# Performance work log

Measured on AMD Instinct MI355X. Metric: run time of the kernel, lower is better.

The kernel has to match this reference:

```python
import jax, jax.numpy as jnp
import numpy as np

D_MODEL = 2048
NUM_HEADS = 16
HEAD_DIM = D_MODEL // NUM_HEADS
LAYER_IDX = 0
NUM_LAYERS = 13
REINIT_LAMBDA = 0.8


def setup_inputs() -> dict:
    key = jax.random.key(0)
    ks = jax.random.split(key, 8)
    B, S = 2, 2048
    x = jax.random.normal(ks[0], (B, S, D_MODEL), dtype=jnp.float32)
    init = 1.0 / np.sqrt(D_MODEL)
    def w(k):
        return jax.random.uniform(k, (D_MODEL, D_MODEL), dtype=jnp.float32, minval=-init, maxval=init)
    lam_init = REINIT_LAMBDA * ((LAYER_IDX + 1) / NUM_LAYERS)
    return {
        "x": x,
        "q1_w": w(ks[1]), "k1_w": w(ks[2]),
        "q2_w": w(ks[3]), "k2_w": w(ks[4]),
        "v_w": w(ks[5]), "o_w": w(ks[6]),
        "lambda_param": jnp.full((NUM_HEADS,), lam_init, dtype=jnp.float32),
    }


def _heads(t, B, S):
    # [B, S, D] -> [B, H, S, Dh]
    return t.reshape(B, S, NUM_HEADS, HEAD_DIM).transpose(0, 2, 1, 3)


def reference(x, q1_w, k1_w, q2_w, k2_w, v_w, o_w, lambda_param):
    B, S, _ = x.shape
    # nn.Linear(bias=False): y = x @ W.T, W is [out, in]
    q1 = _heads(x @ q1_w.T, B, S)
    k1 = _heads(x @ k1_w.T, B, S)
    q2 = _heads(x @ q2_w.T, B, S)
    k2 = _heads(x @ k2_w.T, B, S)
    v = _heads(x @ v_w.T, B, S)
    scale = jnp.sqrt(jnp.float32(HEAD_DIM))
    attn1 = jax.nn.softmax(jnp.einsum('bhqd,bhkd->bhqk', q1, k1) / scale, axis=-1)
    attn2 = jax.nn.softmax(jnp.einsum('bhqd,bhkd->bhqk', q2, k2) / scale, axis=-1)
    lam = lambda_param.reshape(1, NUM_HEADS, 1, 1)
    out = jnp.einsum('bhqk,bhkd->bhqd', attn1 - lam * attn2, v)
    out = out.transpose(0, 2, 1, 3).reshape(B, S, D_MODEL)
    return out @ o_w.T
```

## Files before the change

kernel.cpp:

```cpp
#include <hip/hip_runtime.h>
#include <hip/hip_bf16.h>
#include <stdint.h>

typedef __bf16 bf16_t;
typedef __bf16 bf16x8 __attribute__((ext_vector_type(8)));
typedef float f32x4 __attribute__((ext_vector_type(4)));

#define D_MODEL 2048
#define SEQ     2048
#define NHEADS  16
#define HDIM    128
#define BATCH   2
#define NTOK    (BATCH * SEQ)
#define NELEM   ((size_t)BATCH * SEQ * D_MODEL)
#define D2      ((size_t)D_MODEL * D_MODEL)

__global__ void __launch_bounds__(256)
cvt7_kernel(const float* __restrict__ x,
            const float* __restrict__ w0, const float* __restrict__ w1,
            const float* __restrict__ w2, const float* __restrict__ w3,
            const float* __restrict__ w4, const float* __restrict__ w5,
            bf16_t* __restrict__ xb, bf16_t* __restrict__ wb) {
  const int y = blockIdx.y;
  const float* srcs[7] = {x, w0, w1, w2, w3, w4, w5};
  const float* src = srcs[y];
  bf16_t* dst = (y == 0) ? xb : wb + (size_t)(y - 1) * D2;
  const size_t n = (y == 0) ? NELEM : D2;
  const size_t base = ((size_t)blockIdx.x * 256 + threadIdx.x) * 8;
  if (base >= n) return;
  f32x4 lo = *(const f32x4*)(src + base);
  f32x4 hi = *(const f32x4*)(src + base + 4);
  union { bf16x8 v; bf16_t h[8]; } u;
#pragma unroll
  for (int j = 0; j < 4; j++) {
    u.h[j]     = (bf16_t)lo[j];
    u.h[j + 4] = (bf16_t)hi[j];
  }
  *(bf16x8*)(dst + base) = u.v;
}

__device__ __forceinline__ void async_load16(const void* g, void* l) {
  __builtin_amdgcn_global_load_lds(
      (const __attribute__((address_space(1))) void*)g,
      (__attribute__((address_space(3))) void*)l, 16, 0, 0);
}

template <int TRANS, typename TC>
__device__ __forceinline__ void gemm_tile_body(const bf16_t* __restrict__ A,
                                               const bf16_t* __restrict__ W,
                                               TC* __restrict__ C) {
  extern __shared__ char smem[];
  bf16_t* As = (bf16_t*)smem;
  bf16_t* Bs = (bf16_t*)smem + 128 * 32;
  const int K = D_MODEL, N = D_MODEL;
  const int tid  = threadIdx.x;
  const int wave = tid >> 6, lane = tid & 63;
  const int quad = lane >> 4, l16 = lane & 15;
  const int tm = blockIdx.x * 128, tn = blockIdx.y * 128;
  const int wm = (wave & 1) * 64, wn = (wave >> 1) * 64;

  f32x4 acc[4][4];
#pragma unroll
  for (int i = 0; i < 4; i++)
#pragma unroll
    for (int j = 0; j < 4; j++) acc[i][j] = (f32x4){0.f, 0.f, 0.f, 0.f};

  const int srow = lane >> 2;
  const int scol = (lane & 3) * 8;

  for (int k0 = 0; k0 < K; k0 += 32) {
    __syncthreads();
#pragma unroll
    for (int i = 0; i < 2; i++) {
      const int rbase = (i * 4 + wave) * 16;
      async_load16(A + (size_t)(tm + rbase + srow) * K + k0 + scol, As + rbase * 32);
      async_load16(W + (size_t)(tn + rbase + srow) * K + k0 + scol, Bs + rbase * 32);
    }
    __syncthreads();

    bf16x8 af[4], bfr[4];
#pragma unroll
    for (int i = 0; i < 4; i++)
      af[i] = *(const bf16x8*)(As + (wm + i * 16 + l16) * 32 + quad * 8);
#pragma unroll
    for (int j = 0; j < 4; j++)
      bfr[j] = *(const bf16x8*)(Bs + (wn + j * 16 + l16) * 32 + quad * 8);
#pragma unroll
    for (int i = 0; i < 4; i++)
#pragma unroll
      for (int j = 0; j < 4; j++)
        acc[i][j] = __builtin_amdgcn_mfma_f32_16x16x32_bf16(af[i], bfr[j], acc[i][j], 0, 0, 0);
  }

#pragma unroll
  for (int i = 0; i < 4; i++) {
    const int r0 = wm + i * 16 + quad * 4;
#pragma unroll
    for (int j = 0; j < 4; j++) {
      const int c = tn + wn + j * 16 + l16;
      if constexpr (TRANS) {
        const int m = tm + r0;
        const int b = m >> 11;
        const int s = m & (SEQ - 1);
        union { bf16_t h[4]; uint2 u2; } p;
#pragma unroll
        for (int r = 0; r < 4; r++) p.h[r] = (bf16_t)acc[i][j][r];
        *(uint2*)((bf16_t*)C + (size_t)(b * D_MODEL + c) * SEQ + s) = p.u2;
      } else {
#pragma unroll
        for (int r = 0; r < 4; r++)
          C[(size_t)(tm + r0 + r) * N + c] = (TC)acc[i][j][r];
      }
    }
  }
}

__global__ void __launch_bounds__(256)
gemm_out_kernel(const bf16_t* __restrict__ A, const bf16_t* __restrict__ W,
                float* __restrict__ C) {
  gemm_tile_body<0, float>(A, W, C);
}

template <int TRANS, typename TC>
__device__ __forceinline__ void gemm256_body(const bf16_t* __restrict__ A,
                                             const bf16_t* __restrict__ W,
                                             TC* __restrict__ C,
                                             const int tm, const int tn) {
  extern __shared__ char smem[];
  constexpr int K = D_MODEL;
  constexpr int NT = K / 64;
  const int tid = threadIdx.x;
  const int wid = tid >> 6, lane = tid & 63;
  const int quad = lane >> 4, l16 = lane & 15;
  const int wm = wid >> 2, wn = wid & 3;

  const int sr = lane >> 2;
  const int sc = (lane & 3) ^ ((lane >> 4) & 2);
  const int rdoff = (l16 * 64 + quad * 16) ^ ((l16 & 8) << 2);

  f32x4 acc[8][4];
#pragma unroll
  for (int i = 0; i < 8; i++)
#pragma unroll
    for (int j = 0; j < 4; j++) acc[i][j] = (f32x4){0.f, 0.f, 0.f, 0.f};

  bf16x8 af[2][4], bfA[2][2], bfB[2][2];

#define STAGE256(P, rowbase, ldsbase, h, t)                                      \
  {                                                                              \
    const bf16_t* _s = (P) + (size_t)((rowbase) + (h) * 128 + wid * 16 + sr) * K \
                           + ((t) * 64 + sc * 8);                                \
    char* _d = smem + (ldsbase) + (h) * 16384 + wid * 2048;                      \
    async_load16(_s, _d);                                                        \
    async_load16(_s + 32, _d + 1024);                                            \
  }

#define LDA256(c, rh)                                                            \
  _Pragma("unroll") for (int ks = 0; ks < 2; ks++)                               \
  _Pragma("unroll") for (int j = 0; j < 4; j++)                                  \
      af[ks][j] = *(const bf16x8*)(smem + (c) * 65536 +                          \
                  ((wm * 8 + (rh) * 4 + j) * 2 + ks) * 1024 + rdoff);

#define LDB256(c, dst, cf0)                                                      \
  _Pragma("unroll") for (int ks = 0; ks < 2; ks++)                               \
  _Pragma("unroll") for (int j = 0; j < 2; j++)                                  \
      dst[ks][j] = *(const bf16x8*)(smem + (c) * 65536 + 32768 +                 \
                   ((wn * 4 + (cf0) + j) * 2 + ks) * 1024 + rdoff);

#define MFMA16(rh, bfr, cb)                                                      \
  _Pragma("unroll") for (int j = 0; j < 4; j++)                                  \
  _Pragma("unroll") for (int cf = 0; cf < 2; cf++)                               \
  _Pragma("unroll") for (int ks = 0; ks < 2; ks++)                               \
      acc[(rh) * 4 + j][(cb) + cf] = __builtin_amdgcn_mfma_f32_16x16x32_bf16(    \
          af[ks][j], bfr[ks][cf], acc[(rh) * 4 + j][(cb) + cf], 0, 0, 0);

#define BAR256() __builtin_amdgcn_s_barrier()
#define LGKM0()                                                                  \
  { asm volatile("s_waitcnt lgkmcnt(0)" ::: "memory");                           \
    __builtin_amdgcn_sched_barrier(0); }
#define VMW4()                                                                   \
  { asm volatile("s_waitcnt vmcnt(4)" ::: "memory");                             \
    __builtin_amdgcn_sched_barrier(0); }
#define VMW0()                                                                   \
  { asm volatile("s_waitcnt vmcnt(0)" ::: "memory");                             \
    __builtin_amdgcn_sched_barrier(0); }

  STAGE256(A, tm, 0,     0, 0); STAGE256(A, tm, 0,     1, 0);
  STAGE256(W, tn, 32768, 0, 0); STAGE256(W, tn, 32768, 1, 0);
  STAGE256(W, tn, 98304, 0, 1); STAGE256(W, tn, 98304, 1, 1);
  VMW4();
  BAR256();

  for (int it = 0; it < NT / 2; ++it) {
    const int kt = 2 * it;
    const int t2 = (kt + 2 < NT) ? kt + 2 : 0;
    const int t3 = (kt + 3 < NT) ? kt + 3 : 0;

    LDA256(0, 0); LDB256(0, bfA, 0);
    STAGE256(A, tm, 65536, 0, kt + 1);
    BAR256(); LGKM0();
    __builtin_amdgcn_s_setprio(1); MFMA16(0, bfA, 0); __builtin_amdgcn_s_setprio(0);
    BAR256();
    LDB256(0, bfB, 2);
    STAGE256(A, tm, 65536, 1, kt + 1);
    BAR256(); LGKM0();
    __builtin_amdgcn_s_setprio(1); MFMA16(0, bfB, 2); __builtin_amdgcn_s_setprio(0);
    BAR256();
    LDA256(0, 1);
    STAGE256(W, tn, 32768, 0, t2);
    BAR256(); LGKM0();
    __builtin_amdgcn_s_setprio(1); MFMA16(1, bfA, 0); __builtin_amdgcn_s_setprio(0);
    BAR256();
    STAGE256(W, tn, 32768, 1, t2);
    BAR256();
    __builtin_amdgcn_s_setprio(1); MFMA16(1, bfB, 2); __builtin_amdgcn_s_setprio(0);
    VMW4();
    BAR256();
    LDA256(1, 0); LDB256(1, bfA, 0);
    STAGE256(A, tm, 0, 0, t2);
    BAR256(); LGKM0();
    __builtin_amdgcn_s_setprio(1); MFMA16(0, bfA, 0); __builtin_amdgcn_s_setprio(0);
    BAR256();
    LDB256(1, bfB, 2);
    STAGE256(A, tm, 0, 1, t2);
    BAR256(); LGKM0();
    __builtin_amdgcn_s_setprio(1); MFMA16(0, bfB, 2); __builtin_amdgcn_s_setprio(0);
    BAR256();
    LDA256(1, 1);
    STAGE256(W, tn, 98304, 0, t3);
    BAR256(); LGKM0();
    __builtin_amdgcn_s_setprio(1); MFMA16(1, bfA, 0); __builtin_amdgcn_s_setprio(0);
    BAR256();
    STAGE256(W, tn, 98304, 1, t3);
    BAR256();
    __builtin_amdgcn_s_setprio(1); MFMA16(1, bfB, 2); __builtin_amdgcn_s_setprio(0);
    VMW4();
    BAR256();
  }
  VMW0();

#pragma unroll
  for (int rf = 0; rf < 8; rf++) {
    const int r0 = wm * 128 + rf * 16 + quad * 4;
#pragma unroll
    for (int cf = 0; cf < 4; cf++) {
      const int c = tn + wn * 64 + cf * 16 + l16;
      if constexpr (TRANS) {
        const int m = tm + r0;
        const int b = m >> 11;
        const int s = m & (SEQ - 1);
        union { bf16_t h[4]; uint2 u2; } p;
#pragma unroll
        for (int r = 0; r < 4; r++) p.h[r] = (bf16_t)acc[rf][cf][r];
        *(uint2*)((bf16_t*)C + (size_t)(b * D_MODEL + c) * SEQ + s) = p.u2;
      } else {
#pragma unroll
        for (int r = 0; r < 4; r++)
          C[(size_t)(tm + r0 + r) * D_MODEL + c] = (TC)acc[rf][cf][r];
      }
    }
  }
#undef STAGE256
#undef LDA256
#undef LDB256
#undef MFMA16
#undef BAR256
#undef LGKM0
#undef VMW4
#undef VMW0
}

__global__ void __launch_bounds__(512, 2)
proj5_kernel(const bf16_t* __restrict__ xb, const bf16_t* __restrict__ wb,
             bf16_t* __restrict__ q1, bf16_t* __restrict__ k1,
             bf16_t* __restrict__ q2, bf16_t* __restrict__ k2,
             bf16_t* __restrict__ vt) {
  const int g = blockIdx.y;
  const int orig = blockIdx.x;
  const int wg = (orig & 7) * 16 + (orig >> 3);
  const int tm = (wg & 15) * 256;
  const int tn = (wg >> 4) * 256;
  const bf16_t* w = wb + (size_t)g * D2;
  if (g == 4) {
    gemm256_body<1, bf16_t>(xb, w, vt, tm, tn);
  } else {
    bf16_t* o = (g == 0) ? q1 : (g == 1) ? k1 : (g == 2) ? q2 : k2;
    gemm256_body<0, bf16_t>(xb, w, o, tm, tn);
  }
}

__global__ void __launch_bounds__(256, 3)
diff_attn_kernel(const bf16_t* __restrict__ q1g, const bf16_t* __restrict__ k1g,
                 const bf16_t* __restrict__ q2g, const bf16_t* __restrict__ k2g,
                 const bf16_t* __restrict__ vtg, const float* __restrict__ lamg,
                 bf16_t* __restrict__ outg) {
  const int blk = blockIdx.x;
  const int xcd = blk & 7;
  const int idx = blk >> 3;
  const int bh  = xcd * 4 + (idx >> 5);
  const int qt  = idx & 31;
  const int b = bh >> 4, h = bh & 15;
  const int tid = threadIdx.x, wave = tid >> 6, lane = tid & 63;
  const int quad = lane >> 4, l16 = lane & 15;
  const int stream = wave >> 1;
  const int wq     = wave & 1;
  const int q0 = qt * 64 + wq * 32;

  __shared__ char smem_all[49152];
  bf16_t* K1s = (bf16_t*)smem_all;
  bf16_t* K2s = (bf16_t*)(smem_all + 16384);
  bf16_t* Vs  = (bf16_t*)(smem_all + 32768);

  const bf16_t* k1p = k1g + (size_t)b * SEQ * D_MODEL + h * HDIM;
  const bf16_t* k2p = k2g + (size_t)b * SEQ * D_MODEL + h * HDIM;
  const bf16_t* vtp = vtg + ((size_t)b * D_MODEL + h * HDIM) * SEQ;
  const bf16_t* qp  = (stream ? q2g : q1g) +
                      ((size_t)b * SEQ + q0) * D_MODEL + h * HDIM;
  const bf16_t* Ksp = stream ? K2s : K1s;

  bf16x8 aqa[4], aqb[4];
#pragma unroll
  for (int c = 0; c < 4; c++) {
    aqa[c] = *(const bf16x8*)(qp + (size_t)l16 * D_MODEL + c * 32 + quad * 8);
    aqb[c] = *(const bf16x8*)(qp + (size_t)(16 + l16) * D_MODEL + c * 32 + quad * 8);
  }

  f32x4 Oa[8], Ob[8];
#pragma unroll
  for (int n = 0; n < 8; n++) {
    Oa[n] = (f32x4){0.f, 0.f, 0.f, 0.f};
    Ob[n] = (f32x4){0.f, 0.f, 0.f, 0.f};
  }
  float la = 0.f, lb = 0.f;

  const float c2 = 0.0883883476483184f * 1.4426950408889634f;

  const int k_r  = lane >> 4;
  const int k_p  = lane & 15;
  const int v_r  = lane >> 3;
  const int v_p  = lane & 7;

  for (int kt = 0; kt < SEQ; kt += 64) {
    __syncthreads();
#pragma unroll
    for (int i = 0; i < 4; i++) {
      const int krb = wave * 16 + i * 4;
      const int kr  = krb + k_r;
      const int kkey = (((kr >> 2) & 3) << 3) | (((kr >> 4) & 1) << 2) |
                       (kr & 3) | (kr & 32);
      const int kg = k_p ^ (kr & 7);
      async_load16(k1p + (size_t)(kt + kkey) * D_MODEL + kg * 8, K1s + krb * 128);
      async_load16(k2p + (size_t)(kt + kkey) * D_MODEL + kg * 8, K2s + krb * 128);
      const int vrb = wave * 32 + i * 8;
      const int vr  = vrb + v_r;
      const int vg  = v_p ^ (vr & 7);
      async_load16(vtp + (size_t)vr * SEQ + kt + vg * 8, Vs + vrb * 64);
    }
    __syncthreads();

    const int xsw = l16 & 7;

    f32x4 sa[4], sb[4];
#pragma unroll
    for (int s = 0; s < 4; s++) {
      sa[s] = (f32x4){0.f, 0.f, 0.f, 0.f};
      sb[s] = (f32x4){0.f, 0.f, 0.f, 0.f};
    }
#pragma unroll
    for (int c = 0; c < 4; c++) {
      const int pos = ((c * 4 + quad) ^ xsw) * 8;
#pragma unroll
      for (int s = 0; s < 4; s++) {
        bf16x8 f = *(const bf16x8*)(Ksp + (s * 16 + l16) * 128 + pos);
        sa[s] = __builtin_amdgcn_mfma_f32_16x16x32_bf16(f, aqa[c], sa[s], 0, 0, 0);
        sb[s] = __builtin_amdgcn_mfma_f32_16x16x32_bf16(f, aqb[c], sb[s], 0, 0, 0);
      }
    }

    union { bf16x8 v; bf16_t h[8]; } pa[2], pb[2];
#pragma unroll
    for (int s = 0; s < 4; s++) {
#pragma unroll
      for (int r = 0; r < 4; r++) {
        const float ea = __builtin_amdgcn_exp2f(sa[s][r] * c2);
        const float eb = __builtin_amdgcn_exp2f(sb[s][r] * c2);
        pa[s >> 1].h[(s & 1) * 4 + r] = (bf16_t)ea; la += ea;
        pb[s >> 1].h[(s & 1) * 4 + r] = (bf16_t)eb; lb += eb;
      }
    }

#pragma unroll
    for (int half = 0; half < 2; half++) {
      const int vpos = ((half * 4 + quad) ^ xsw) * 8;
#pragma unroll
      for (int n = 0; n < 8; n++) {
        bf16x8 vf = *(const bf16x8*)(Vs + (n * 16 + l16) * 64 + vpos);
        Oa[n] = __builtin_amdgcn_mfma_f32_16x16x32_bf16(pa[half].v, vf, Oa[n], 0, 0, 0);
        Ob[n] = __builtin_amdgcn_mfma_f32_16x16x32_bf16(pb[half].v, vf, Ob[n], 0, 0, 0);
      }
    }
  }

  la += __shfl_xor(la, 16); la += __shfl_xor(la, 32);
  lb += __shfl_xor(lb, 16); lb += __shfl_xor(lb, 32);

  __syncthreads();
  float* xfer = (float*)smem_all;

  if (stream == 1) {
    const float lam = lamg[h];
    const float ia = lam / la, ib = lam / lb;
    float iao[4], ibo[4];
#pragma unroll
    for (int r = 0; r < 4; r++) {
      iao[r] = __shfl(ia, quad * 4 + r, 16);
      ibo[r] = __shfl(ib, quad * 4 + r, 16);
    }
#pragma unroll
    for (int r = 0; r < 4; r++)
#pragma unroll
      for (int n = 0; n < 8; n++) {
        xfer[(wq * 32 + quad * 4 + r) * 128 + n * 16 + l16] = Oa[n][r] * iao[r];
        xfer[(wq * 32 + 16 + quad * 4 + r) * 128 + n * 16 + l16] = Ob[n][r] * ibo[r];
      }
  }
  __syncthreads();
  if (stream == 0) {
    const float ia = 1.f / la, ib = 1.f / lb;
    float iao[4], ibo[4];
#pragma unroll
    for (int r = 0; r < 4; r++) {
      iao[r] = __shfl(ia, quad * 4 + r, 16);
      ibo[r] = __shfl(ib, quad * 4 + r, 16);
    }
    bf16_t* op = outg + ((size_t)b * SEQ + q0) * D_MODEL + h * HDIM;
#pragma unroll
    for (int r = 0; r < 4; r++)
#pragma unroll
      for (int n = 0; n < 8; n++) {
        const float va = Oa[n][r] * iao[r] -
                         xfer[(wq * 32 + quad * 4 + r) * 128 + n * 16 + l16];
        const float vb = Ob[n][r] * ibo[r] -
                         xfer[(wq * 32 + 16 + quad * 4 + r) * 128 + n * 16 + l16];
        op[(size_t)(quad * 4 + r) * D_MODEL + n * 16 + l16] = (bf16_t)va;
        op[(size_t)(16 + quad * 4 + r) * D_MODEL + n * 16 + l16] = (bf16_t)vb;
      }
  }
}

extern "C" void kernel_launch(void* const* d_in, const int* in_sizes, int n_in,
                              void* d_out, int out_size, void* d_ws, size_t ws_size,
                              hipStream_t stream) {
  const float* x   = (const float*)d_in[0];
  const float* wq1 = (const float*)d_in[1];
  const float* wk1 = (const float*)d_in[2];
  const float* wq2 = (const float*)d_in[3];
  const float* wk2 = (const float*)d_in[4];
  const float* wv  = (const float*)d_in[5];
  const float* wo  = (const float*)d_in[6];
  const float* lam = (const float*)d_in[7];

  bf16_t* ws = (bf16_t*)d_ws;
  bf16_t* q1 = ws + 0 * NELEM;
  bf16_t* k1 = ws + 1 * NELEM;
  bf16_t* q2 = ws + 2 * NELEM;
  bf16_t* k2 = ws + 3 * NELEM;
  bf16_t* vt = ws + 4 * NELEM;
  bf16_t* xb = ws + 5 * NELEM;
  bf16_t* ao = xb;
  bf16_t* wb = ws + 6 * NELEM;

  static bool attr_set = false;
  if (!attr_set) {
    (void)hipFuncSetAttribute(reinterpret_cast<const void*>(proj5_kernel),
                              hipFuncAttributeMaxDynamicSharedMemorySize, 131072);
    attr_set = true;
  }

  cvt7_kernel<<<dim3(4096, 7), dim3(256), 0, stream>>>(
      x, wq1, wk1, wq2, wk2, wv, wo, xb, wb);
  proj5_kernel<<<dim3(128, 5), dim3(512), 131072, stream>>>(
      xb, wb, q1, k1, q2, k2, vt);
  diff_attn_kernel<<<dim3(BATCH * NHEADS * (SEQ / 64)), dim3(256), 0, stream>>>(
      q1, k1, q2, k2, vt, lam, ao);
  gemm_out_kernel<<<dim3(NTOK / 128, D_MODEL / 128), dim3(256), 16384, stream>>>(
      ao, wb + 5 * D2, (float*)d_out);
}
```

Measured before the change: 577.7 us.

## Prefetch next K/V tile into registers while computing current attention tile

Swaps the synchronous async-to-LDS tile loads for a register-staged software pipeline. Each iteration issues global loads for the next K1/K2/V tile into registers before the current tile's MFMA work, then writes them to shared memory after a barrier. Address offsets are hoisted out of the loop. This is meant to hide global-load latency behind compute, at the cost of more registers (12 uint4 per thread) and possibly lower occupancy.

```diff
diff --git a/kernel.cpp b/kernel.cpp
--- a/kernel.cpp
+++ b/kernel.cpp
@@ -340,23 +340,55 @@
   const int v_r  = lane >> 3;
   const int v_p  = lane & 7;
 
+  size_t koffs[4], voffs[4];
+  int kdst[4], vdst[4];
+#pragma unroll
+  for (int i = 0; i < 4; i++) {
+    const int krb = wave * 16 + i * 4;
+    const int kr  = krb + k_r;
+    const int kkey = (((kr >> 2) & 3) << 3) | (((kr >> 4) & 1) << 2) |
+                     (kr & 3) | (kr & 32);
+    const int kg = k_p ^ (kr & 7);
+    koffs[i] = (size_t)kkey * D_MODEL + kg * 8;
+    kdst[i]  = krb * 128 + lane * 8;
+    const int vrb = wave * 32 + i * 8;
+    const int vr  = vrb + v_r;
+    const int vg  = v_p ^ (vr & 7);
+    voffs[i] = (size_t)vr * SEQ + vg * 8;
+    vdst[i]  = vrb * 64 + lane * 8;
+  }
+
+  uint4 rk1[4], rk2[4], rv[4];
+
+#define LOADT(KT)                                                                \
+  {                                                                              \
+    const bf16_t* _k1 = k1p + (size_t)(KT) * D_MODEL;                            \
+    const bf16_t* _k2 = k2p + (size_t)(KT) * D_MODEL;                            \
+    const bf16_t* _vt = vtp + (KT);                                              \
+    _Pragma("unroll") for (int i = 0; i < 4; i++) {                              \
+      rk1[i] = *(const uint4*)(_k1 + koffs[i]);                                  \
+      rk2[i] = *(const uint4*)(_k2 + koffs[i]);                                  \
+      rv[i]  = *(const uint4*)(_vt + voffs[i]);                                  \
+    }                                                                            \
+    __builtin_amdgcn_sched_barrier(0);                                           \
+  }
+
+#define STORET()                                                                 \
+  {                                                                              \
+    _Pragma("unroll") for (int i = 0; i < 4; i++) {                              \
+      *(uint4*)(K1s + kdst[i]) = rk1[i];                                         \
+      *(uint4*)(K2s + kdst[i]) = rk2[i];                                         \
+      *(uint4*)(Vs  + vdst[i]) = rv[i];                                          \
+    }                                                                            \
+  }
+
+  LOADT(0);
+  STORET();
+  __syncthreads();
+
   for (int kt = 0; kt < SEQ; kt += 64) {
-    __syncthreads();
-#pragma unroll
-    for (int i = 0; i < 4; i++) {
-      const int krb = wave * 16 + i * 4;
-      const int kr  = krb + k_r;
-      const int kkey = (((kr >> 2) & 3) << 3) | (((kr >> 4) & 1) << 2) |
-                       (kr & 3) | (kr & 32);
-      const int kg = k_p ^ (kr & 7);
-      async_load16(k1p + (size_t)(kt + kkey) * D_MODEL + kg * 8, K1s + krb * 128);
-      async_load16(k2p + (size_t)(kt + kkey) * D_MODEL + kg * 8, K2s + krb * 128);
-      const int vrb = wave * 32 + i * 8;
-      const int vr  = vrb + v_r;
-      const int vg  = v_p ^ (vr & 7);
-      async_load16(vtp + (size_t)vr * SEQ + kt + vg * 8, Vs + vrb * 64);
-    }
-    __syncthreads();
+    const int nxt = kt + 64;
+    if (nxt < SEQ) LOADT(nxt);
 
     const int xsw = l16 & 7;
 
@@ -399,7 +431,15 @@
         Ob[n] = __builtin_amdgcn_mfma_f32_16x16x32_bf16(pb[half].v, vf, Ob[n], 0, 0, 0);
       }
     }
-  }
+
+    __syncthreads();
+    if (nxt < SEQ) {
+      STORET();
+      __syncthreads();
+    }
+  }
+#undef LOADT
+#undef STORET
 
   la += __shfl_xor(la, 16); la += __shfl_xor(la, 32);
   lb += __shfl_xor(lb, 16); lb += __shfl_xor(lb, 32);
```

Result: slower. 1.269 ms (+119.6%).

## Double-buffer K tiles and prefetch V in diff attention loop

Applied to the files above, without the earlier changes.

Restructures the attention key loop so K1/K2 tiles are double-buffered and the next tile's loads are issued before the current QK^T compute. V loads are issued after the PV MFMAs and overlap the next iteration's QK step, with explicit vmcnt waits and barriers replacing the two full syncs. MFMA sections also get raised wave priority. LDS use grows from 48KB to 80KB, so occupancy drops from 3 to 2 blocks per CU, trading latency hiding across blocks for overlap within a block.

```diff
diff --git a/kernel.cpp b/kernel.cpp
--- a/kernel.cpp
+++ b/kernel.cpp
@@ -289,7 +289,7 @@
   }
 }
 
-__global__ void __launch_bounds__(256, 3)
+__global__ void __launch_bounds__(256, 2)
 diff_attn_kernel(const bf16_t* __restrict__ q1g, const bf16_t* __restrict__ k1g,
                  const bf16_t* __restrict__ q2g, const bf16_t* __restrict__ k2g,
                  const bf16_t* __restrict__ vtg, const float* __restrict__ lamg,
@@ -306,17 +306,17 @@
   const int wq     = wave & 1;
   const int q0 = qt * 64 + wq * 32;
 
-  __shared__ char smem_all[49152];
-  bf16_t* K1s = (bf16_t*)smem_all;
-  bf16_t* K2s = (bf16_t*)(smem_all + 16384);
-  bf16_t* Vs  = (bf16_t*)(smem_all + 32768);
+  __shared__ char smem_all[81920];
+  bf16_t* K1b = (bf16_t*)smem_all;
+  bf16_t* K2b = (bf16_t*)(smem_all + 32768);
+  bf16_t* Vs  = (bf16_t*)(smem_all + 65536);
 
   const bf16_t* k1p = k1g + (size_t)b * SEQ * D_MODEL + h * HDIM;
   const bf16_t* k2p = k2g + (size_t)b * SEQ * D_MODEL + h * HDIM;
   const bf16_t* vtp = vtg + ((size_t)b * D_MODEL + h * HDIM) * SEQ;
   const bf16_t* qp  = (stream ? q2g : q1g) +
                       ((size_t)b * SEQ + q0) * D_MODEL + h * HDIM;
-  const bf16_t* Ksp = stream ? K2s : K1s;
+  const bf16_t* Ksb = stream ? K2b : K1b;
 
   bf16x8 aqa[4], aqb[4];
 #pragma unroll
@@ -340,24 +340,45 @@
   const int v_r  = lane >> 3;
   const int v_p  = lane & 7;
 
-  for (int kt = 0; kt < SEQ; kt += 64) {
-    __syncthreads();
-#pragma unroll
-    for (int i = 0; i < 4; i++) {
-      const int krb = wave * 16 + i * 4;
-      const int kr  = krb + k_r;
-      const int kkey = (((kr >> 2) & 3) << 3) | (((kr >> 4) & 1) << 2) |
-                       (kr & 3) | (kr & 32);
-      const int kg = k_p ^ (kr & 7);
-      async_load16(k1p + (size_t)(kt + kkey) * D_MODEL + kg * 8, K1s + krb * 128);
-      async_load16(k2p + (size_t)(kt + kkey) * D_MODEL + kg * 8, K2s + krb * 128);
-      const int vrb = wave * 32 + i * 8;
-      const int vr  = vrb + v_r;
-      const int vg  = v_p ^ (vr & 7);
-      async_load16(vtp + (size_t)vr * SEQ + kt + vg * 8, Vs + vrb * 64);
-    }
-    __syncthreads();
-
+#define STAGE_K(KT, BUF)                                                         \
+  { _Pragma("unroll") for (int i = 0; i < 4; i++) {                              \
+      const int krb = wave * 16 + i * 4;                                         \
+      const int kr  = krb + k_r;                                                 \
+      const int kkey = (((kr >> 2) & 3) << 3) | (((kr >> 4) & 1) << 2) |         \
+                       (kr & 3) | (kr & 32);                                     \
+      const int kg = k_p ^ (kr & 7);                                             \
+      async_load16(k1p + (size_t)((KT) + kkey) * D_MODEL + kg * 8,               \
+                   K1b + (BUF) * 8192 + krb * 128);                              \
+      async_load16(k2p + (size_t)((KT) + kkey) * D_MODEL + kg * 8,               \
+                   K2b + (BUF) * 8192 + krb * 128);                              \
+  } }
+
+#define STAGE_V(KT)                                                              \
+  { _Pragma("unroll") for (int i = 0; i < 4; i++) {                              \
+      const int vrb = wave * 32 + i * 8;                                         \
+      const int vr  = vrb + v_r;                                                 \
+      const int vg  = v_p ^ (vr & 7);                                            \
+      async_load16(vtp + (size_t)vr * SEQ + (KT) + vg * 8, Vs + vrb * 64);       \
+  } }
+
+#define VMW(N)                                                                   \
+  { asm volatile("s_waitcnt vmcnt(" #N ")" ::: "memory");                        \
+    __builtin_amdgcn_sched_barrier(0); }
+#define BARR()                                                                   \
+  { __builtin_amdgcn_s_barrier();                                                \
+    __builtin_amdgcn_sched_barrier(0); }
+
+  STAGE_K(0, 0);
+  STAGE_V(0);
+  VMW(0); BARR();
+
+  for (int t = 0; t < SEQ / 64; ++t) {
+    const int ktn = (t < SEQ / 64 - 1) ? (t + 1) * 64 : 0;
+    STAGE_K(ktn, (t + 1) & 1);
+    VMW(12);
+    BARR();
+
+    const bf16_t* Kc = Ksb + (t & 1) * 8192;
     const int xsw = l16 & 7;
 
     f32x4 sa[4], sb[4];
@@ -366,16 +387,18 @@
       sa[s] = (f32x4){0.f, 0.f, 0.f, 0.f};
       sb[s] = (f32x4){0.f, 0.f, 0.f, 0.f};
     }
+    __builtin_amdgcn_s_setprio(1);
 #pragma unroll
     for (int c = 0; c < 4; c++) {
       const int pos = ((c * 4 + quad) ^ xsw) * 8;
 #pragma unroll
       for (int s = 0; s < 4; s++) {
-        bf16x8 f = *(const bf16x8*)(Ksp + (s * 16 + l16) * 128 + pos);
+        bf16x8 f = *(const bf16x8*)(Kc + (s * 16 + l16) * 128 + pos);
         sa[s] = __builtin_amdgcn_mfma_f32_16x16x32_bf16(f, aqa[c], sa[s], 0, 0, 0);
         sb[s] = __builtin_amdgcn_mfma_f32_16x16x32_bf16(f, aqb[c], sb[s], 0, 0, 0);
       }
     }
+    __builtin_amdgcn_s_setprio(0);
 
     union { bf16x8 v; bf16_t h[8]; } pa[2], pb[2];
 #pragma unroll
@@ -389,6 +412,10 @@
       }
     }
 
+    VMW(8);
+    BARR();
+
+    __builtin_amdgcn_s_setprio(1);
 #pragma unroll
     for (int half = 0; half < 2; half++) {
       const int vpos = ((half * 4 + quad) ^ xsw) * 8;
@@ -399,7 +426,15 @@
         Ob[n] = __builtin_amdgcn_mfma_f32_16x16x32_bf16(pb[half].v, vf, Ob[n], 0, 0, 0);
       }
     }
-  }
+    __builtin_amdgcn_s_setprio(0);
+
+    BARR();
+    STAGE_V(ktn);
+  }
+#undef STAGE_K
+#undef STAGE_V
+#undef VMW
+#undef BARR
 
   la += __shfl_xor(la, 16); la += __shfl_xor(la, 32);
   lb += __shfl_xor(lb, 16); lb += __shfl_xor(lb, 32);
```

After: 509.4 us. -11.8%, faster.
